# Performance work log

Hardware: AMD Instinct MI355X
Metric: run time of the kernel (lower is better)

The kernel has to match this reference:

```python
import jax, jax.numpy as jnp
import numpy as np

G, NB, C, K, R, S = 5, 5, 64, 3, 8, 2   # n_groups, n_blocks, n_feats, kernel, reduction, scale
MOCO = 256


def setup_inputs() -> dict:
    key = jax.random.key(0)
    ks = iter(jax.random.split(key, 32))
    def rn(shape, s=0.02):
        return jax.random.normal(next(ks), shape, jnp.float32) * s
    return {
        "x": jax.random.normal(next(ks), (16, 3, 64, 64), jnp.float32),
        "k_v": jax.random.normal(next(ks), (16, MOCO), jnp.float32),
        "head_w": rn((C, 3, K, K)), "head_b": rn((C,)),
        "comp_w": rn((C, MOCO)),
        # DA_conv params, stacked over [group, block, which-of-2]
        "da_kw1": rn((G, NB, 2, C, C)),
        "da_kw2": rn((G, NB, 2, C * K * K, C)),
        "da_cw": rn((G, NB, 2, C, C)), "da_cb": rn((G, NB, 2, C)),
        "ca_w1": rn((G, NB, 2, C // R, C)), "ca_w2": rn((G, NB, 2, C, C // R)),
        # DAB plain 3x3 convs (conv1, conv2)
        "dab_cw": rn((G, NB, 2, C, C, K, K)), "dab_cb": rn((G, NB, 2, C)),
        # per-group tail conv, body tail conv, upsampler, final conv
        "grp_w": rn((G, C, C, K, K)), "grp_b": rn((G, C)),
        "body_w": rn((C, C, K, K)), "body_b": rn((C,)),
        "up_w": rn((C * S * S, C, K, K)), "up_b": rn((C * S * S,)),
        "tail_w": rn((3, C, K, K)), "tail_b": rn((3,)),
    }


def lrelu(x):
    return jax.nn.leaky_relu(x, 0.1)


def conv2d(x, w, b):
    p = (K - 1) // 2
    y = jax.lax.conv_general_dilated(x, w, (1, 1), [(p, p), (p, p)],
                                     dimension_numbers=("NCHW", "OIHW", "NCHW"))
    return y + b[None, :, None, None]


def da_conv(x, kv, kw1, kw2, cw, cb, caw1, caw2):
    # x: [B,C,H,W], kv: [B,C]
    B, Ch, H, W = x.shape
    # per-sample, per-channel dynamic KxK kernel (torch: groups=B*C depthwise conv)
    ker = (lrelu(kv @ kw1.T) @ kw2.T).reshape(B, Ch, K, K)
    p = (K - 1) // 2
    xp = jnp.pad(x, ((0, 0), (0, 0), (p, p), (p, p)))
    out = jnp.zeros_like(x)
    for i in range(K):
        for j in range(K):
            out = out + ker[:, :, i, j, None, None] * xp[:, :, i:i + H, j:j + W]
    out = lrelu(out)
    # 1x1 conv (with bias)
    out = jnp.einsum("bchw,oc->bohw", out, cw) + cb[None, :, None, None]
    # CA gate on kv (two bias-free 1x1 convs on 1x1 spatial == matmuls)
    att = jax.nn.sigmoid(lrelu(kv @ caw1.T) @ caw2.T)  # [B,C]
    return out + x * att[:, :, None, None]


def pixel_shuffle(t, r):
    B, Ct, H, W = t.shape
    c = Ct // (r * r)
    return t.reshape(B, c, r, r, H, W).transpose(0, 1, 4, 2, 5, 3).reshape(B, c, H * r, W * r)


def _forward(x, k_v, head_w, head_b, comp_w, da_kw1, da_kw2, da_cw, da_cb,
             ca_w1, ca_w2, dab_cw, dab_cb, grp_w, grp_b, body_w, body_b,
             up_w, up_b, tail_w, tail_b):
    kv = lrelu(k_v @ comp_w.T)            # compress: [B, C]
    x0 = conv2d(x, head_w, head_b)        # head
    res = x0
    for g in range(G):                    # DAGs
        gin = res
        for n in range(NB):               # DABs
            bin_ = res
            out = lrelu(da_conv(res, kv, da_kw1[g, n, 0], da_kw2[g, n, 0],
                                da_cw[g, n, 0], da_cb[g, n, 0], ca_w1[g, n, 0], ca_w2[g, n, 0]))
            out = lrelu(conv2d(out, dab_cw[g, n, 0], dab_cb[g, n, 0]))
            out = lrelu(da_conv(out, kv, da_kw1[g, n, 1], da_kw2[g, n, 1],
                                da_cw[g, n, 1], da_cb[g, n, 1], ca_w1[g, n, 1], ca_w2[g, n, 1]))
            res = conv2d(out, dab_cw[g, n, 1], dab_cb[g, n, 1]) + bin_
        res = conv2d(res, grp_w[g], grp_b[g]) + gin
    res = conv2d(res, body_w, body_b) + x0
    t = pixel_shuffle(conv2d(res, up_w, up_b), S)   # Upsampler (scale=2)
    return conv2d(t, tail_w, tail_b)


def reference(x, k_v, head_w, head_b, comp_w, da_kw1, da_kw2, da_cw, da_cb,
              ca_w1, ca_w2, dab_cw, dab_cb, grp_w, grp_b, body_w, body_b,
              up_w, up_b, tail_w, tail_b):
    return _forward(x, k_v, head_w, head_b, comp_w, da_kw1, da_kw2, da_cw, da_cb,
                    ca_w1, ca_w2, dab_cw, dab_cb, grp_w, grp_b, body_w, body_b,
                    up_w, up_b, tail_w, tail_b)
```

## Files before the change

kernel.cpp:

```cpp
#include <hip/hip_runtime.h>
#include <math.h>

#define DEV __device__ __forceinline__

DEV float lrelu_f(float v) { return v > 0.f ? v : 0.1f * v; }

DEV unsigned short f2bf(float f) {
    unsigned u = __builtin_bit_cast(unsigned, f);
    unsigned r = u + 0x7FFFu + ((u >> 16) & 1u);
    return (unsigned short)(r >> 16);
}

DEV float bf2f(unsigned short s) {
    return __builtin_bit_cast(float, (unsigned)s << 16);
}

typedef __attribute__((ext_vector_type(8))) short bh8;
typedef __attribute__((ext_vector_type(16))) float f16acc;

#define MFMA32(acc, a, b) acc = __builtin_amdgcn_mfma_f32_32x32x16_bf16(a, b, acc, 0, 0, 0)

__global__ void transpose_w(const float* __restrict__ src, float* __restrict__ dst,
                            int L, int O, int KK) {
    int idx = blockIdx.x * 256 + threadIdx.x;
    int tot = L * O * KK;
    if (idx >= tot) return;
    int l = idx / (O * KK);
    int r = idx - l * (O * KK);
    int o = r / KK;
    int k = r - o * KK;
    dst[((size_t)l * KK + k) * O + o] = src[idx];
}

__global__ void pack3x3(const float* __restrict__ src, unsigned short* __restrict__ dst, int L) {
    int idx = blockIdx.x * 256 + threadIdx.x;
    if (idx >= L * 4608) return;
    int l = idx / 4608;
    int r = idx - l * 4608;
    int c = r >> 7;
    int rr = r & 127;
    int nt = rr >> 6, lane = rr & 63;
    int o = nt * 32 + (lane & 31);
    int kg = lane >> 5;
    unsigned short v[8];
#pragma unroll
    for (int j = 0; j < 8; ++j) {
        int k = c * 16 + kg * 8 + j;
        int t = k >> 6, cin = k & 63;
        v[j] = f2bf(src[(((size_t)l * 64 + o) * 64 + cin) * 9 + t]);
    }
    uint4 u;
    u.x = v[0] | ((unsigned)v[1] << 16);
    u.y = v[2] | ((unsigned)v[3] << 16);
    u.z = v[4] | ((unsigned)v[5] << 16);
    u.w = v[6] | ((unsigned)v[7] << 16);
    *(uint4*)(dst + (size_t)idx * 8) = u;
}

__global__ void pack_da(const float* __restrict__ src, unsigned short* __restrict__ dst, int L) {
    int idx = blockIdx.x * 256 + threadIdx.x;
    if (idx >= L * 512) return;
    int l = idx >> 9;
    int r = idx & 511;
    int c = r >> 7;
    int rr = r & 127;
    int nt = rr >> 6, lane = rr & 63;
    int o = nt * 32 + (lane & 31);
    int kg = lane >> 5;
    unsigned short v[8];
#pragma unroll
    for (int j = 0; j < 8; ++j) {
        int cin = c * 16 + kg * 8 + j;
        v[j] = f2bf(src[((size_t)l * 64 + o) * 64 + cin]);
    }
    uint4 u;
    u.x = v[0] | ((unsigned)v[1] << 16);
    u.y = v[2] | ((unsigned)v[3] << 16);
    u.z = v[4] | ((unsigned)v[5] << 16);
    u.w = v[6] | ((unsigned)v[7] << 16);
    *(uint4*)(dst + (size_t)idx * 8) = u;
}

__global__ void pack_up(const float* __restrict__ src, unsigned short* __restrict__ dst) {
    int idx = blockIdx.x * 256 + threadIdx.x;
    if (idx >= 18432) return;
    int c = idx >> 9;
    int nt = (idx >> 6) & 7;
    int lane = idx & 63;
    int o = nt * 32 + (lane & 31);
    int kg = lane >> 5;
    unsigned short v[8];
#pragma unroll
    for (int j = 0; j < 8; ++j) {
        int k = c * 16 + kg * 8 + j;
        int t = k >> 6, cin = k & 63;
        v[j] = f2bf(src[((size_t)o * 64 + cin) * 9 + t]);
    }
    uint4 u;
    u.x = v[0] | ((unsigned)v[1] << 16);
    u.y = v[2] | ((unsigned)v[3] << 16);
    u.z = v[4] | ((unsigned)v[5] << 16);
    u.w = v[6] | ((unsigned)v[7] << 16);
    *(uint4*)(dst + (size_t)idx * 8) = u;
}

__global__ void pack_tail(const float* __restrict__ src, unsigned short* __restrict__ dst) {
    int idx = blockIdx.x * 256 + threadIdx.x;
    if (idx >= 2304) return;
    int c = idx >> 6;
    int lane = idx & 63;
    int o = lane & 31;
    int kg = lane >> 5;
    unsigned short v[8];
#pragma unroll
    for (int j = 0; j < 8; ++j) {
        int k = c * 16 + kg * 8 + j;
        int t = k >> 6, cin = k & 63;
        v[j] = (o < 3) ? f2bf(src[((size_t)o * 64 + cin) * 9 + t]) : (unsigned short)0;
    }
    uint4 u;
    u.x = v[0] | ((unsigned)v[1] << 16);
    u.y = v[2] | ((unsigned)v[3] << 16);
    u.z = v[4] | ((unsigned)v[5] << 16);
    u.w = v[6] | ((unsigned)v[7] << 16);
    *(uint4*)(dst + (size_t)idx * 8) = u;
}

__global__ void kv_kernel(const float* __restrict__ kvin, const float* __restrict__ comp_w,
                          float* __restrict__ kv) {
    int b = blockIdx.x, c = threadIdx.x;
    const float* a = kvin + b * 256;
    const float* w = comp_w + c * 256;
    float s = 0.f;
    for (int m = 0; m < 256; ++m) s += a[m] * w[m];
    kv[b * 64 + c] = lrelu_f(s);
}

__global__ void kerprep(const float* __restrict__ kv, const float* __restrict__ kw1,
                        const float* __restrict__ kw2, const float* __restrict__ caw1,
                        const float* __restrict__ caw2, float* __restrict__ ker_all,
                        float* __restrict__ att_all) {
    int l = blockIdx.x >> 4;
    int b = blockIdx.x & 15;
    int c = threadIdx.x;
    __shared__ float kvb[64];
    __shared__ float t1[64];
    __shared__ float a1[8];
    kvb[c] = kv[b * 64 + c];
    __syncthreads();
    {
        const float* w1 = kw1 + (size_t)l * 4096 + c * 64;
        float s = 0.f;
        for (int j = 0; j < 64; ++j) s += kvb[j] * w1[j];
        t1[c] = lrelu_f(s);
    }
    if (c < 8) {
        const float* cw1 = caw1 + (size_t)l * 512 + c * 64;
        float s = 0.f;
        for (int j = 0; j < 64; ++j) s += kvb[j] * cw1[j];
        a1[c] = lrelu_f(s);
    }
    __syncthreads();
    const float* w2 = kw2 + (size_t)l * 576 * 64;
    for (int t = 0; t < 9; ++t) {
        const float* row = w2 + (size_t)(c * 9 + t) * 64;
        float s = 0.f;
        for (int j = 0; j < 64; ++j) s += t1[j] * row[j];
        ker_all[(((size_t)l * 16 + b) * 9 + t) * 64 + c] = s;
    }
    {
        const float* c2 = caw2 + (size_t)l * 512 + c * 8;
        float s = 0.f;
        for (int r = 0; r < 8; ++r) s += a1[r] * c2[r];
        att_all[((size_t)l * 16 + b) * 64 + c] = 1.f / (1.f + expf(-s));
    }
}

__global__ __launch_bounds__(256) void head_conv(const float* __restrict__ x,
                                                 const float* __restrict__ wt,
                                                 const float* __restrict__ bias,
                                                 float* __restrict__ x0,
                                                 float* __restrict__ res) {
    int t = threadIdx.x;
    int co = t & 63, q = t >> 6;
    int bid = blockIdx.x;
    int b = bid >> 7;
    int rem = bid & 127;
    int y = rem >> 1;
    int xs = (rem & 1) * 32 + q * 8;

    float bv = bias[co];
    float acc[8];
#pragma unroll
    for (int p = 0; p < 8; ++p) acc[p] = bv;

    int coff[10];
    bool cok[10];
#pragma unroll
    for (int i = 0; i < 10; ++i) {
        int col = xs - 1 + i;
        cok[i] = (col >= 0) && (col < 64);
        coff[i] = cok[i] ? col : 0;
    }
    for (int cin = 0; cin < 3; ++cin) {
#pragma unroll
        for (int ky = 0; ky < 3; ++ky) {
            int row = y + ky - 1;
            bool rok = (row >= 0) && (row < 64);
            const float* rp = x + ((size_t)(b * 3 + cin) * 64 + (rok ? row : 0)) * 64;
            float v[10];
#pragma unroll
            for (int i = 0; i < 10; ++i) v[i] = (rok && cok[i]) ? rp[coff[i]] : 0.f;
            const float* wp = wt + ((cin * 3 + ky) * 3) * 64 + co;
            float w0 = wp[0], w1 = wp[64], w2 = wp[128];
#pragma unroll
            for (int p = 0; p < 8; ++p) acc[p] += w0 * v[p] + w1 * v[p + 1] + w2 * v[p + 2];
        }
    }
    size_t ob = (((size_t)b * 64 + y) * 64 + xs) * 64 + co;
#pragma unroll
    for (int p = 0; p < 8; ++p) {
        x0[ob + (size_t)p * 64] = acc[p];
        res[ob + (size_t)p * 64] = acc[p];
    }
}

__global__ __launch_bounds__(256) void conv3x3_mfma(const float* __restrict__ in,
                                                    const unsigned short* __restrict__ wp,
                                                    const float* __restrict__ bias,
                                                    const float* __restrict__ resid,
                                                    float* __restrict__ out, int act) {
    __shared__ unsigned short sm[180 * 72];
    int tid = threadIdx.x;
    int bid = blockIdx.x;
    int b = bid >> 5;
    int rem = bid & 31;
    int ty = rem >> 2, tx = rem & 3;
    const float* inb = in + (size_t)b * 262144;

    for (int i = tid; i < 2880; i += 256) {
        int px = i >> 4, c4 = i & 15;
        int hy = px / 18, hx = px - hy * 18;
        int row = ty * 8 + hy - 1, col = tx * 16 + hx - 1;
        float4 v = make_float4(0.f, 0.f, 0.f, 0.f);
        if (row >= 0 && row < 64 && col >= 0 && col < 64)
            v = *(const float4*)(inb + (((size_t)row * 64 + col) * 64 + c4 * 4));
        uint2 u;
        u.x = f2bf(v.x) | ((unsigned)f2bf(v.y) << 16);
        u.y = f2bf(v.z) | ((unsigned)f2bf(v.w) << 16);
        *(uint2*)&sm[px * 72 + c4 * 4] = u;
    }
    __syncthreads();

    int lane = tid & 63, w = tid >> 6;
    int l31 = lane & 31, kg8 = (lane >> 5) * 8;
    int p0 = w * 32 + l31;
    int ly0 = p0 >> 4, lx0 = p0 & 15;

    f16acc a0 = {0,0,0,0,0,0,0,0,0,0,0,0,0,0,0,0};
    f16acc a1 = a0;

#pragma unroll
    for (int t = 0; t < 9; ++t) {
        int tyt = t / 3, txt = t - tyt * 3;
        int base = ((ly0 + tyt) * 18 + lx0 + txt) * 72 + kg8;
#pragma unroll
        for (int cc = 0; cc < 4; ++cc) {
            int c = t * 4 + cc;
            bh8 A = *(const bh8*)&sm[base + cc * 16];
            bh8 B0 = *(const bh8*)&wp[((size_t)(c * 2 + 0) * 64 + lane) * 8];
            bh8 B1 = *(const bh8*)&wp[((size_t)(c * 2 + 1) * 64 + lane) * 8];
            MFMA32(a0, A, B0);
            MFMA32(a1, A, B1);
        }
    }

    float bias0 = bias[l31], bias1 = bias[32 + l31];
    int hi = lane >> 5;
    size_t outb = (size_t)b * 262144;
#pragma unroll
    for (int r = 0; r < 16; ++r) {
        int rowm = (r & 3) + 8 * (r >> 2) + 4 * hi;
        int m = w * 32 + rowm;
        int gy = ty * 8 + (m >> 4), gx = tx * 16 + (m & 15);
        size_t i0 = outb + (((size_t)gy * 64 + gx) * 64);
        float v0 = a0[r] + bias0, v1 = a1[r] + bias1;
        if (resid) {
            v0 += resid[i0 + l31];
            v1 += resid[i0 + 32 + l31];
        }
        if (act) { v0 = lrelu_f(v0); v1 = lrelu_f(v1); }
        out[i0 + l31] = v0;
        out[i0 + 32 + l31] = v1;
    }
}

__global__ __launch_bounds__(256) void da_mfma(const float* __restrict__ in,
                                               const unsigned short* __restrict__ wp,
                                               const float* __restrict__ cb,
                                               const float* __restrict__ kerT,
                                               const float* __restrict__ attv,
                                               float* __restrict__ out) {
    __shared__ unsigned short sm[(180 + 128) * 72];
    const int MIDOFF = 180 * 72;
    int tid = threadIdx.x;
    int bid = blockIdx.x;
    int b = bid >> 5;
    int rem = bid & 31;
    int ty = rem >> 2, tx = rem & 3;
    const float* inb = in + (size_t)b * 262144;

    for (int i = tid; i < 2880; i += 256) {
        int px = i >> 4, c4 = i & 15;
        int hy = px / 18, hx = px - hy * 18;
        int row = ty * 8 + hy - 1, col = tx * 16 + hx - 1;
        float4 v = make_float4(0.f, 0.f, 0.f, 0.f);
        if (row >= 0 && row < 64 && col >= 0 && col < 64)
            v = *(const float4*)(inb + (((size_t)row * 64 + col) * 64 + c4 * 4));
        uint2 u;
        u.x = f2bf(v.x) | ((unsigned)f2bf(v.y) << 16);
        u.y = f2bf(v.z) | ((unsigned)f2bf(v.w) << 16);
        *(uint2*)&sm[px * 72 + c4 * 4] = u;
    }
    __syncthreads();

    {
        int c = tid & 63, q = tid >> 6;
        const float* kb = kerT + (size_t)b * 576;
        float k[9];
#pragma unroll
        for (int t = 0; t < 9; ++t) k[t] = kb[t * 64 + c];
#pragma unroll
        for (int rr = 0; rr < 2; ++rr) {
            int ly = q * 2 + rr;
            float m[16];
#pragma unroll
            for (int xx = 0; xx < 16; ++xx) m[xx] = 0.f;
#pragma unroll
            for (int ky = 0; ky < 3; ++ky) {
                int hr = ly + ky;
                float v[18];
#pragma unroll
                for (int i = 0; i < 18; ++i) v[i] = bf2f(sm[(hr * 18 + i) * 72 + c]);
                float k0 = k[ky * 3], k1 = k[ky * 3 + 1], k2 = k[ky * 3 + 2];
#pragma unroll
                for (int xx = 0; xx < 16; ++xx) m[xx] += k0 * v[xx] + k1 * v[xx + 1] + k2 * v[xx + 2];
            }
#pragma unroll
            for (int xx = 0; xx < 16; ++xx)
                sm[MIDOFF + (ly * 16 + xx) * 72 + c] = f2bf(lrelu_f(m[xx]));
        }
    }
    __syncthreads();

    int lane = tid & 63, w = tid >> 6;
    int l31 = lane & 31, kg8 = (lane >> 5) * 8;
    int base = MIDOFF + (w * 32 + l31) * 72 + kg8;

    f16acc a0 = {0,0,0,0,0,0,0,0,0,0,0,0,0,0,0,0};
    f16acc a1 = a0;
#pragma unroll
    for (int cc = 0; cc < 4; ++cc) {
        bh8 A = *(const bh8*)&sm[base + cc * 16];
        bh8 B0 = *(const bh8*)&wp[((size_t)(cc * 2 + 0) * 64 + lane) * 8];
        bh8 B1 = *(const bh8*)&wp[((size_t)(cc * 2 + 1) * 64 + lane) * 8];
        MFMA32(a0, A, B0);
        MFMA32(a1, A, B1);
    }

    float cb0 = cb[l31], cb1 = cb[32 + l31];
    float at0 = attv[b * 64 + l31], at1 = attv[b * 64 + 32 + l31];
    int hi = lane >> 5;
    size_t outb = (size_t)b * 262144;
#pragma unroll
    for (int r = 0; r < 16; ++r) {
        int rowm = (r & 3) + 8 * (r >> 2) + 4 * hi;
        int m = w * 32 + rowm;
        int gy = ty * 8 + (m >> 4), gx = tx * 16 + (m & 15);
        size_t i0 = outb + (((size_t)gy * 64 + gx) * 64);
        float v0 = a0[r] + cb0 + in[i0 + l31] * at0;
        float v1 = a1[r] + cb1 + in[i0 + 32 + l31] * at1;
        out[i0 + l31] = lrelu_f(v0);
        out[i0 + 32 + l31] = lrelu_f(v1);
    }
}

__global__ __launch_bounds__(256) void up_mfma(const float* __restrict__ in,
                                               const unsigned short* __restrict__ wp,
                                               const float* __restrict__ bias,
                                               float* __restrict__ shuf) {
    __shared__ unsigned short sm[100 * 72];
    int tid = threadIdx.x;
    int bid = blockIdx.x;
    int b = bid >> 6;
    int t6 = bid & 63;
    int ty = t6 >> 3, tx = t6 & 7;
    const float* inb = in + (size_t)b * 262144;

    for (int i = tid; i < 1600; i += 256) {
        int px = i >> 4, c4 = i & 15;
        int hy = px / 10, hx = px - hy * 10;
        int row = ty * 8 + hy - 1, col = tx * 8 + hx - 1;
        float4 v = make_float4(0.f, 0.f, 0.f, 0.f);
        if (row >= 0 && row < 64 && col >= 0 && col < 64)
            v = *(const float4*)(inb + (((size_t)row * 64 + col) * 64 + c4 * 4));
        uint2 u;
        u.x = f2bf(v.x) | ((unsigned)f2bf(v.y) << 16);
        u.y = f2bf(v.z) | ((unsigned)f2bf(v.w) << 16);
        *(uint2*)&sm[px * 72 + c4 * 4] = u;
    }
    __syncthreads();

    int lane = tid & 63, w = tid >> 6;
    int l31 = lane & 31, kg8 = (lane >> 5) * 8;
    int ly0 = l31 >> 3, lx0 = l31 & 7;

    f16acc a00 = {0,0,0,0,0,0,0,0,0,0,0,0,0,0,0,0};
    f16acc a01 = a00, a10 = a00, a11 = a00;

#pragma unroll
    for (int t = 0; t < 9; ++t) {
        int tyt = t / 3, txt = t - tyt * 3;
        int base0 = ((ly0 + tyt) * 10 + lx0 + txt) * 72 + kg8;
        int base1 = base0 + 2880;
#pragma unroll
        for (int cc = 0; cc < 4; ++cc) {
            int c = t * 4 + cc;
            bh8 A0 = *(const bh8*)&sm[base0 + cc * 16];
            bh8 A1 = *(const bh8*)&sm[base1 + cc * 16];
            bh8 B0 = *(const bh8*)&wp[((size_t)(c * 8 + w * 2 + 0) * 64 + lane) * 8];
            bh8 B1 = *(const bh8*)&wp[((size_t)(c * 8 + w * 2 + 1) * 64 + lane) * 8];
            MFMA32(a00, A0, B0);
            MFMA32(a01, A0, B1);
            MFMA32(a10, A1, B0);
            MFMA32(a11, A1, B1);
        }
    }

    int co0 = w * 64 + l31, co1 = co0 + 32;
    float bias0 = bias[co0], bias1 = bias[co1];
    int ch0 = co0 >> 2, r10 = (co0 >> 1) & 1, r20 = co0 & 1;
    int ch1 = co1 >> 2, r11 = (co1 >> 1) & 1, r21 = co1 & 1;
    int hi = lane >> 5;
#pragma unroll
    for (int r = 0; r < 16; ++r) {
        int rowm = (r & 3) + 8 * (r >> 2) + 4 * hi;
#pragma unroll
        for (int mt = 0; mt < 2; ++mt) {
            int m = mt * 32 + rowm;
            int y = ty * 8 + (m >> 3), x = tx * 8 + (m & 7);
            float va = (mt == 0) ? a00[r] : a10[r];
            float vb = (mt == 0) ? a01[r] : a11[r];
            shuf[(((size_t)b * 128 + 2 * y + r10) * 128 + 2 * x + r20) * 64 + ch0] = va + bias0;
            shuf[(((size_t)b * 128 + 2 * y + r11) * 128 + 2 * x + r21) * 64 + ch1] = vb + bias1;
        }
    }
}

__global__ __launch_bounds__(256) void tail_mfma(const float* __restrict__ shuf,
                                                 const unsigned short* __restrict__ wp,
                                                 const float* __restrict__ bias,
                                                 float* __restrict__ outp) {
    __shared__ unsigned short sm[324 * 72];
    int tid = threadIdx.x;
    int bid = blockIdx.x;
    int b = bid >> 6;
    int rem = bid & 63;
    int ty = rem >> 3, tx = rem & 7;
    const float* sb = shuf + (size_t)b * 128 * 128 * 64;

    for (int i = tid; i < 5184; i += 256) {
        int px = i >> 4, c4 = i & 15;
        int hy = px / 18, hx = px - hy * 18;
        int row = ty * 16 + hy - 1, col = tx * 16 + hx - 1;
        float4 v = make_float4(0.f, 0.f, 0.f, 0.f);
        if (row >= 0 && row < 128 && col >= 0 && col < 128)
            v = *(const float4*)(sb + (((size_t)row * 128 + col) * 64 + c4 * 4));
        uint2 u;
        u.x = f2bf(v.x) | ((unsigned)f2bf(v.y) << 16);
        u.y = f2bf(v.z) | ((unsigned)f2bf(v.w) << 16);
        *(uint2*)&sm[px * 72 + c4 * 4] = u;
    }
    __syncthreads();

    int lane = tid & 63, w = tid >> 6;
    int l31 = lane & 31, kg8 = (lane >> 5) * 8;
    int mbase = w * 64;
    int p0 = mbase + l31;
    int ly0 = p0 >> 4, lx0 = p0 & 15;

    f16acc a0 = {0,0,0,0,0,0,0,0,0,0,0,0,0,0,0,0};
    f16acc a1 = a0;

#pragma unroll
    for (int t = 0; t < 9; ++t) {
        int tyt = t / 3, txt = t - tyt * 3;
        int base0 = ((ly0 + tyt) * 18 + lx0 + txt) * 72 + kg8;
        int base1 = base0 + 2592;
#pragma unroll
        for (int cc = 0; cc < 4; ++cc) {
            int c = t * 4 + cc;
            bh8 A0 = *(const bh8*)&sm[base0 + cc * 16];
            bh8 A1 = *(const bh8*)&sm[base1 + cc * 16];
            bh8 B = *(const bh8*)&wp[((size_t)c * 64 + lane) * 8];
            MFMA32(a0, A0, B);
            MFMA32(a1, A1, B);
        }
    }

    if (l31 < 3) {
        float bv = bias[l31];
        int hi = lane >> 5;
        size_t ob = ((size_t)b * 3 + l31) * 16384;
#pragma unroll
        for (int r = 0; r < 16; ++r) {
            int rowm = (r & 3) + 8 * (r >> 2) + 4 * hi;
            int m0 = mbase + rowm;
            int gy0 = ty * 16 + (m0 >> 4), gx0 = tx * 16 + (m0 & 15);
            outp[ob + (size_t)gy0 * 128 + gx0] = a0[r] + bv;
            int m1 = m0 + 32;
            int gy1 = ty * 16 + (m1 >> 4), gx1 = tx * 16 + (m1 & 15);
            outp[ob + (size_t)gy1 * 128 + gx1] = a1[r] + bv;
        }
    }
}

extern "C" void kernel_launch(void* const* d_in, const int* in_sizes, int n_in,
                              void* d_out, int out_size, void* d_ws, size_t ws_size,
                              hipStream_t stream) {
    const float* x      = (const float*)d_in[0];
    const float* k_v    = (const float*)d_in[1];
    const float* head_w = (const float*)d_in[2];
    const float* head_b = (const float*)d_in[3];
    const float* comp_w = (const float*)d_in[4];
    const float* da_kw1 = (const float*)d_in[5];
    const float* da_kw2 = (const float*)d_in[6];
    const float* da_cw  = (const float*)d_in[7];
    const float* da_cb  = (const float*)d_in[8];
    const float* ca_w1  = (const float*)d_in[9];
    const float* ca_w2  = (const float*)d_in[10];
    const float* dab_cw = (const float*)d_in[11];
    const float* dab_cb = (const float*)d_in[12];
    const float* grp_w  = (const float*)d_in[13];
    const float* grp_b  = (const float*)d_in[14];
    const float* body_w = (const float*)d_in[15];
    const float* body_b = (const float*)d_in[16];
    const float* up_w   = (const float*)d_in[17];
    const float* up_b   = (const float*)d_in[18];
    const float* tail_w = (const float*)d_in[19];
    const float* tail_b = (const float*)d_in[20];

    char* base = (char*)d_ws;
    auto alloc = [&](size_t bytes) -> char* {
        char* p = base;
        base += (bytes + 255) & ~(size_t)255;
        return p;
    };
    unsigned short* wp_dab  = (unsigned short*)alloc((size_t)50 * 36864 * 2);
    unsigned short* wp_grp  = (unsigned short*)alloc((size_t)5 * 36864 * 2);
    unsigned short* wp_body = (unsigned short*)alloc((size_t)36864 * 2);
    unsigned short* wp_up   = (unsigned short*)alloc((size_t)147456 * 2);
    unsigned short* wp_da   = (unsigned short*)alloc((size_t)50 * 4096 * 2);
    unsigned short* wp_tail = (unsigned short*)alloc((size_t)18432 * 2);
    float* wT_head = (float*)alloc(1728 * 4);
    float* kvbuf   = (float*)alloc(1024 * 4);
    float* ker_all = (float*)alloc((size_t)460800 * 4);
    float* att_all = (float*)alloc((size_t)51200 * 4);
    const size_t ACT = (size_t)16 * 64 * 64 * 64;
    float* x0  = (float*)alloc(ACT * 4);
    float* b0  = (float*)alloc(ACT * 4);
    float* b1  = (float*)alloc(ACT * 4);
    float* b2  = (float*)alloc(ACT * 4);
    float* t0b = (float*)alloc(ACT * 4);
    float* t1b = (float*)alloc(ACT * 4);
    float* shuf = (float*)alloc((size_t)16 * 128 * 128 * 64 * 4);

    pack3x3<<<900, 256, 0, stream>>>(dab_cw, wp_dab, 50);
    pack3x3<<<90, 256, 0, stream>>>(grp_w, wp_grp, 5);
    pack3x3<<<18, 256, 0, stream>>>(body_w, wp_body, 1);
    pack_da<<<100, 256, 0, stream>>>(da_cw, wp_da, 50);
    pack_up<<<72, 256, 0, stream>>>(up_w, wp_up);
    pack_tail<<<9, 256, 0, stream>>>(tail_w, wp_tail);
    transpose_w<<<7, 256, 0, stream>>>(head_w, wT_head, 1, 64, 27);

    kv_kernel<<<16, 64, 0, stream>>>(k_v, comp_w, kvbuf);
    kerprep<<<800, 64, 0, stream>>>(kvbuf, da_kw1, da_kw2, ca_w1, ca_w2, ker_all, att_all);

    head_conv<<<2048, 256, 0, stream>>>(x, wT_head, head_b, x0, b0);

    for (int g = 0; g < 5; ++g) {
        float* rin = b0;
        for (int n = 0; n < 5; ++n) {
            int l0 = (g * 5 + n) * 2, l1 = l0 + 1;
            da_mfma<<<512, 256, 0, stream>>>(rin, wp_da + (size_t)l0 * 4096,
                                             da_cb + (size_t)l0 * 64, ker_all + (size_t)l0 * 9216,
                                             att_all + (size_t)l0 * 1024, t0b);
            conv3x3_mfma<<<512, 256, 0, stream>>>(t0b, wp_dab + (size_t)l0 * 36864,
                                                  dab_cb + (size_t)l0 * 64, nullptr, t1b, 1);
            da_mfma<<<512, 256, 0, stream>>>(t1b, wp_da + (size_t)l1 * 4096,
                                             da_cb + (size_t)l1 * 64, ker_all + (size_t)l1 * 9216,
                                             att_all + (size_t)l1 * 1024, t0b);
            float* rout = (rin == b1) ? b2 : b1;
            conv3x3_mfma<<<512, 256, 0, stream>>>(t0b, wp_dab + (size_t)l1 * 36864,
                                                  dab_cb + (size_t)l1 * 64, rin, rout, 0);
            rin = rout;
        }
        float* gout = (rin == b1) ? b2 : b1;
        conv3x3_mfma<<<512, 256, 0, stream>>>(rin, wp_grp + (size_t)g * 36864,
                                              grp_b + (size_t)g * 64, b0, gout, 0);
        float* ob0 = b0;
        b0 = gout;
        b1 = ob0;
        b2 = rin;
    }
    conv3x3_mfma<<<512, 256, 0, stream>>>(b0, wp_body, body_b, x0, b1, 0);

    up_mfma<<<1024, 256, 0, stream>>>(b1, wp_up, up_b, shuf);
    tail_mfma<<<1024, 256, 0, stream>>>(shuf, wp_tail, tail_b, (float*)d_out);
}
```

Measured before the change: 1.887 ms.

## Store intermediate activations as bf16 and enlarge conv3x3 tiles to 16x16

Intermediate activations between kernels are now written and read as bf16, with fp32 copies kept only for residual streams. This halves global memory traffic and removes the per-load fp32-to-bf16 conversion in every conv, DA, upsample and tail kernel. conv3x3_mfma now computes a 16x16 tile per block with four accumulators per wave, so each B-fragment load is reused twice and half as many blocks are launched. The DA kernel also stages its 1x1 weights in LDS. Rounding intermediates to bf16 adds precision loss, and fewer blocks may lower occupancy.

```diff
diff --git a/kernel.cpp b/kernel.cpp
--- a/kernel.cpp
+++ b/kernel.cpp
@@ -180,7 +180,8 @@
                                                  const float* __restrict__ wt,
                                                  const float* __restrict__ bias,
                                                  float* __restrict__ x0,
-                                                 float* __restrict__ res) {
+                                                 float* __restrict__ res,
+                                                 unsigned short* __restrict__ resS) {
     int t = threadIdx.x;
     int co = t & 63, q = t >> 6;
     int bid = blockIdx.x;
@@ -222,60 +223,179 @@
     for (int p = 0; p < 8; ++p) {
         x0[ob + (size_t)p * 64] = acc[p];
         res[ob + (size_t)p * 64] = acc[p];
-    }
-}
-
-__global__ __launch_bounds__(256) void conv3x3_mfma(const float* __restrict__ in,
+        resS[ob + (size_t)p * 64] = f2bf(acc[p]);
+    }
+}
+
+__global__ __launch_bounds__(256) void conv3x3_mfma(const unsigned short* __restrict__ in,
                                                     const unsigned short* __restrict__ wp,
                                                     const float* __restrict__ bias,
-                                                    const float* __restrict__ resid,
-                                                    float* __restrict__ out, int act) {
+                                                    const float* __restrict__ residF,
+                                                    float* __restrict__ outF,
+                                                    unsigned short* __restrict__ outB,
+                                                    int act) {
+    __shared__ unsigned short sm[324 * 72];
+    int tid = threadIdx.x;
+    int bid = blockIdx.x;
+    int b = bid >> 4, ty = (bid >> 2) & 3, tx = bid & 3;
+    const unsigned short* inb = in + (size_t)b * 262144;
+
+    for (int i = tid; i < 2592; i += 256) {
+        int px = i >> 3, c8 = i & 7;
+        int hy = px / 18, hx = px - hy * 18;
+        int row = ty * 16 + hy - 1, col = tx * 16 + hx - 1;
+        uint4 u = make_uint4(0u, 0u, 0u, 0u);
+        if (row >= 0 && row < 64 && col >= 0 && col < 64)
+            u = *(const uint4*)(inb + (((size_t)row * 64 + col) * 64 + c8 * 8));
+        *(uint4*)&sm[px * 72 + c8 * 8] = u;
+    }
+    __syncthreads();
+
+    int lane = tid & 63, w = tid >> 6;
+    int l31 = lane & 31, kg8 = (lane >> 5) * 8;
+    int mbase = w * 64;
+    int p0 = mbase + l31;
+    int ly0 = p0 >> 4, lx0 = p0 & 15;
+
+    f16acc a00 = {0,0,0,0,0,0,0,0,0,0,0,0,0,0,0,0};
+    f16acc a01 = a00, a10 = a00, a11 = a00;
+
+#pragma unroll
+    for (int t = 0; t < 9; ++t) {
+        int tyt = t / 3, txt = t - tyt * 3;
+        int base0 = ((ly0 + tyt) * 18 + lx0 + txt) * 72 + kg8;
+        int base1 = base0 + 2592;
+#pragma unroll
+        for (int cc = 0; cc < 4; ++cc) {
+            int c = t * 4 + cc;
+            bh8 A0 = *(const bh8*)&sm[base0 + cc * 16];
+            bh8 A1 = *(const bh8*)&sm[base1 + cc * 16];
+            bh8 B0 = *(const bh8*)&wp[((size_t)(c * 2 + 0) * 64 + lane) * 8];
+            bh8 B1 = *(const bh8*)&wp[((size_t)(c * 2 + 1) * 64 + lane) * 8];
+            MFMA32(a00, A0, B0);
+            MFMA32(a01, A0, B1);
+            MFMA32(a10, A1, B0);
+            MFMA32(a11, A1, B1);
+        }
+    }
+
+    float bias0 = bias[l31], bias1 = bias[32 + l31];
+    int hi = lane >> 5;
+    size_t outb = (size_t)b * 262144;
+#pragma unroll
+    for (int r = 0; r < 16; ++r) {
+        int rowm = (r & 3) + 8 * (r >> 2) + 4 * hi;
+        int m0 = mbase + rowm;
+        int gy0 = ty * 16 + (m0 >> 4), gx0 = tx * 16 + (m0 & 15);
+        size_t i0 = outb + (((size_t)gy0 * 64 + gx0) * 64);
+        int m1 = m0 + 32;
+        int gy1 = ty * 16 + (m1 >> 4), gx1 = tx * 16 + (m1 & 15);
+        size_t i1 = outb + (((size_t)gy1 * 64 + gx1) * 64);
+        float v00 = a00[r] + bias0, v01 = a01[r] + bias1;
+        float v10 = a10[r] + bias0, v11 = a11[r] + bias1;
+        if (residF) {
+            v00 += residF[i0 + l31];
+            v01 += residF[i0 + 32 + l31];
+            v10 += residF[i1 + l31];
+            v11 += residF[i1 + 32 + l31];
+        }
+        if (act) {
+            v00 = lrelu_f(v00); v01 = lrelu_f(v01);
+            v10 = lrelu_f(v10); v11 = lrelu_f(v11);
+        }
+        if (outF) {
+            outF[i0 + l31] = v00;
+            outF[i0 + 32 + l31] = v01;
+            outF[i1 + l31] = v10;
+            outF[i1 + 32 + l31] = v11;
+        }
+        if (outB) {
+            outB[i0 + l31] = f2bf(v00);
+            outB[i0 + 32 + l31] = f2bf(v01);
+            outB[i1 + l31] = f2bf(v10);
+            outB[i1 + 32 + l31] = f2bf(v11);
+        }
+    }
+}
+
+__global__ __launch_bounds__(256) void da_mfma(const unsigned short* __restrict__ in,
+                                               const unsigned short* __restrict__ wp,
+                                               const float* __restrict__ cb,
+                                               const float* __restrict__ kerT,
+                                               const float* __restrict__ attv,
+                                               unsigned short* __restrict__ out) {
     __shared__ unsigned short sm[180 * 72];
+    __shared__ unsigned short mid[128 * 72];
+    __shared__ unsigned short bds[4096];
     int tid = threadIdx.x;
     int bid = blockIdx.x;
     int b = bid >> 5;
     int rem = bid & 31;
     int ty = rem >> 2, tx = rem & 3;
-    const float* inb = in + (size_t)b * 262144;
-
-    for (int i = tid; i < 2880; i += 256) {
-        int px = i >> 4, c4 = i & 15;
+    const unsigned short* inb = in + (size_t)b * 262144;
+
+    for (int i = tid; i < 1440; i += 256) {
+        int px = i >> 3, c8 = i & 7;
         int hy = px / 18, hx = px - hy * 18;
         int row = ty * 8 + hy - 1, col = tx * 16 + hx - 1;
-        float4 v = make_float4(0.f, 0.f, 0.f, 0.f);
+        uint4 u = make_uint4(0u, 0u, 0u, 0u);
         if (row >= 0 && row < 64 && col >= 0 && col < 64)
-            v = *(const float4*)(inb + (((size_t)row * 64 + col) * 64 + c4 * 4));
-        uint2 u;
-        u.x = f2bf(v.x) | ((unsigned)f2bf(v.y) << 16);
-        u.y = f2bf(v.z) | ((unsigned)f2bf(v.w) << 16);
-        *(uint2*)&sm[px * 72 + c4 * 4] = u;
+            u = *(const uint4*)(inb + (((size_t)row * 64 + col) * 64 + c8 * 8));
+        *(uint4*)&sm[px * 72 + c8 * 8] = u;
+    }
+#pragma unroll
+    for (int i = 0; i < 2; ++i) {
+        int idx = i * 256 + tid;
+        *(uint4*)&bds[idx * 8] = *(const uint4*)&wp[idx * 8];
+    }
+    __syncthreads();
+
+    {
+        int c = tid & 63, q = tid >> 6;
+        const float* kb = kerT + (size_t)b * 576;
+        float k[9];
+#pragma unroll
+        for (int t = 0; t < 9; ++t) k[t] = kb[t * 64 + c];
+#pragma unroll
+        for (int rr = 0; rr < 2; ++rr) {
+            int ly = q * 2 + rr;
+            float m[16];
+#pragma unroll
+            for (int xx = 0; xx < 16; ++xx) m[xx] = 0.f;
+#pragma unroll
+            for (int ky = 0; ky < 3; ++ky) {
+                int hr = ly + ky;
+                float v[18];
+#pragma unroll
+                for (int i = 0; i < 18; ++i) v[i] = bf2f(sm[(hr * 18 + i) * 72 + c]);
+                float k0 = k[ky * 3], k1 = k[ky * 3 + 1], k2 = k[ky * 3 + 2];
+#pragma unroll
+                for (int xx = 0; xx < 16; ++xx) m[xx] += k0 * v[xx] + k1 * v[xx + 1] + k2 * v[xx + 2];
+            }
+#pragma unroll
+            for (int xx = 0; xx < 16; ++xx)
+                mid[(ly * 16 + xx) * 72 + c] = f2bf(lrelu_f(m[xx]));
+        }
     }
     __syncthreads();
 
     int lane = tid & 63, w = tid >> 6;
     int l31 = lane & 31, kg8 = (lane >> 5) * 8;
-    int p0 = w * 32 + l31;
-    int ly0 = p0 >> 4, lx0 = p0 & 15;
+    int base = (w * 32 + l31) * 72 + kg8;
 
     f16acc a0 = {0,0,0,0,0,0,0,0,0,0,0,0,0,0,0,0};
     f16acc a1 = a0;
-
-#pragma unroll
-    for (int t = 0; t < 9; ++t) {
-        int tyt = t / 3, txt = t - tyt * 3;
-        int base = ((ly0 + tyt) * 18 + lx0 + txt) * 72 + kg8;
-#pragma unroll
-        for (int cc = 0; cc < 4; ++cc) {
-            int c = t * 4 + cc;
-            bh8 A = *(const bh8*)&sm[base + cc * 16];
-            bh8 B0 = *(const bh8*)&wp[((size_t)(c * 2 + 0) * 64 + lane) * 8];
-            bh8 B1 = *(const bh8*)&wp[((size_t)(c * 2 + 1) * 64 + lane) * 8];
-            MFMA32(a0, A, B0);
-            MFMA32(a1, A, B1);
-        }
-    }
-
-    float bias0 = bias[l31], bias1 = bias[32 + l31];
+#pragma unroll
+    for (int cc = 0; cc < 4; ++cc) {
+        bh8 A = *(const bh8*)&mid[base + cc * 16];
+        bh8 B0 = *(const bh8*)&bds[((cc * 2 + 0) * 64 + lane) * 8];
+        bh8 B1 = *(const bh8*)&bds[((cc * 2 + 1) * 64 + lane) * 8];
+        MFMA32(a0, A, B0);
+        MFMA32(a1, A, B1);
+    }
+
+    float cb0 = cb[l31], cb1 = cb[32 + l31];
+    float at0 = attv[b * 64 + l31], at1 = attv[b * 64 + 32 + l31];
     int hi = lane >> 5;
     size_t outb = (size_t)b * 262144;
 #pragma unroll
@@ -284,130 +404,33 @@
         int m = w * 32 + rowm;
         int gy = ty * 8 + (m >> 4), gx = tx * 16 + (m & 15);
         size_t i0 = outb + (((size_t)gy * 64 + gx) * 64);
-        float v0 = a0[r] + bias0, v1 = a1[r] + bias1;
-        if (resid) {
-            v0 += resid[i0 + l31];
-            v1 += resid[i0 + 32 + l31];
-        }
-        if (act) { v0 = lrelu_f(v0); v1 = lrelu_f(v1); }
-        out[i0 + l31] = v0;
-        out[i0 + 32 + l31] = v1;
-    }
-}
-
-__global__ __launch_bounds__(256) void da_mfma(const float* __restrict__ in,
-                                               const unsigned short* __restrict__ wp,
-                                               const float* __restrict__ cb,
-                                               const float* __restrict__ kerT,
-                                               const float* __restrict__ attv,
-                                               float* __restrict__ out) {
-    __shared__ unsigned short sm[(180 + 128) * 72];
-    const int MIDOFF = 180 * 72;
-    int tid = threadIdx.x;
-    int bid = blockIdx.x;
-    int b = bid >> 5;
-    int rem = bid & 31;
-    int ty = rem >> 2, tx = rem & 3;
-    const float* inb = in + (size_t)b * 262144;
-
-    for (int i = tid; i < 2880; i += 256) {
-        int px = i >> 4, c4 = i & 15;
-        int hy = px / 18, hx = px - hy * 18;
-        int row = ty * 8 + hy - 1, col = tx * 16 + hx - 1;
-        float4 v = make_float4(0.f, 0.f, 0.f, 0.f);
-        if (row >= 0 && row < 64 && col >= 0 && col < 64)
-            v = *(const float4*)(inb + (((size_t)row * 64 + col) * 64 + c4 * 4));
-        uint2 u;
-        u.x = f2bf(v.x) | ((unsigned)f2bf(v.y) << 16);
-        u.y = f2bf(v.z) | ((unsigned)f2bf(v.w) << 16);
-        *(uint2*)&sm[px * 72 + c4 * 4] = u;
-    }
-    __syncthreads();
-
-    {
-        int c = tid & 63, q = tid >> 6;
-        const float* kb = kerT + (size_t)b * 576;
-        float k[9];
-#pragma unroll
-        for (int t = 0; t < 9; ++t) k[t] = kb[t * 64 + c];
-#pragma unroll
-        for (int rr = 0; rr < 2; ++rr) {
-            int ly = q * 2 + rr;
-            float m[16];
-#pragma unroll
-            for (int xx = 0; xx < 16; ++xx) m[xx] = 0.f;
-#pragma unroll
-            for (int ky = 0; ky < 3; ++ky) {
-                int hr = ly + ky;
-                float v[18];
-#pragma unroll
-                for (int i = 0; i < 18; ++i) v[i] = bf2f(sm[(hr * 18 + i) * 72 + c]);
-                float k0 = k[ky * 3], k1 = k[ky * 3 + 1], k2 = k[ky * 3 + 2];
-#pragma unroll
-                for (int xx = 0; xx < 16; ++xx) m[xx] += k0 * v[xx] + k1 * v[xx + 1] + k2 * v[xx + 2];
-            }
-#pragma unroll
-            for (int xx = 0; xx < 16; ++xx)
-                sm[MIDOFF + (ly * 16 + xx) * 72 + c] = f2bf(lrelu_f(m[xx]));
-        }
-    }
-    __syncthreads();
-
-    int lane = tid & 63, w = tid >> 6;
-    int l31 = lane & 31, kg8 = (lane >> 5) * 8;
-    int base = MIDOFF + (w * 32 + l31) * 72 + kg8;
-
-    f16acc a0 = {0,0,0,0,0,0,0,0,0,0,0,0,0,0,0,0};
-    f16acc a1 = a0;
-#pragma unroll
-    for (int cc = 0; cc < 4; ++cc) {
-        bh8 A = *(const bh8*)&sm[base + cc * 16];
-        bh8 B0 = *(const bh8*)&wp[((size_t)(cc * 2 + 0) * 64 + lane) * 8];
-        bh8 B1 = *(const bh8*)&wp[((size_t)(cc * 2 + 1) * 64 + lane) * 8];
-        MFMA32(a0, A, B0);
-        MFMA32(a1, A, B1);
-    }
-
-    float cb0 = cb[l31], cb1 = cb[32 + l31];
-    float at0 = attv[b * 64 + l31], at1 = attv[b * 64 + 32 + l31];
-    int hi = lane >> 5;
-    size_t outb = (size_t)b * 262144;
-#pragma unroll
-    for (int r = 0; r < 16; ++r) {
-        int rowm = (r & 3) + 8 * (r >> 2) + 4 * hi;
-        int m = w * 32 + rowm;
-        int gy = ty * 8 + (m >> 4), gx = tx * 16 + (m & 15);
-        size_t i0 = outb + (((size_t)gy * 64 + gx) * 64);
-        float v0 = a0[r] + cb0 + in[i0 + l31] * at0;
-        float v1 = a1[r] + cb1 + in[i0 + 32 + l31] * at1;
-        out[i0 + l31] = lrelu_f(v0);
-        out[i0 + 32 + l31] = lrelu_f(v1);
-    }
-}
-
-__global__ __launch_bounds__(256) void up_mfma(const float* __restrict__ in,
+        float v0 = a0[r] + cb0 + bf2f(in[i0 + l31]) * at0;
+        float v1 = a1[r] + cb1 + bf2f(in[i0 + 32 + l31]) * at1;
+        out[i0 + l31] = f2bf(lrelu_f(v0));
+        out[i0 + 32 + l31] = f2bf(lrelu_f(v1));
+    }
+}
+
+__global__ __launch_bounds__(256) void up_mfma(const unsigned short* __restrict__ in,
                                                const unsigned short* __restrict__ wp,
                                                const float* __restrict__ bias,
-                                               float* __restrict__ shuf) {
+                                               unsigned short* __restrict__ shuf) {
     __shared__ unsigned short sm[100 * 72];
     int tid = threadIdx.x;
     int bid = blockIdx.x;
     int b = bid >> 6;
     int t6 = bid & 63;
     int ty = t6 >> 3, tx = t6 & 7;
-    const float* inb = in + (size_t)b * 262144;
-
-    for (int i = tid; i < 1600; i += 256) {
-        int px = i >> 4, c4 = i & 15;
+    const unsigned short* inb = in + (size_t)b * 262144;
+
+    for (int i = tid; i < 800; i += 256) {
+        int px = i >> 3, c8 = i & 7;
         int hy = px / 10, hx = px - hy * 10;
         int row = ty * 8 + hy - 1, col = tx * 8 + hx - 1;
-        float4 v = make_float4(0.f, 0.f, 0.f, 0.f);
+        uint4 u = make_uint4(0u, 0u, 0u, 0u);
         if (row >= 0 && row < 64 && col >= 0 && col < 64)
-            v = *(const float4*)(inb + (((size_t)row * 64 + col) * 64 + c4 * 4));
-        uint2 u;
-        u.x = f2bf(v.x) | ((unsigned)f2bf(v.y) << 16);
-        u.y = f2bf(v.z) | ((unsigned)f2bf(v.w) << 16);
-        *(uint2*)&sm[px * 72 + c4 * 4] = u;
+            u = *(const uint4*)(inb + (((size_t)row * 64 + col) * 64 + c8 * 8));
+        *(uint4*)&sm[px * 72 + c8 * 8] = u;
     }
     __syncthreads();
 
@@ -451,13 +474,13 @@
             int y = ty * 8 + (m >> 3), x = tx * 8 + (m & 7);
             float va = (mt == 0) ? a00[r] : a10[r];
             float vb = (mt == 0) ? a01[r] : a11[r];
-            shuf[(((size_t)b * 128 + 2 * y + r10) * 128 + 2 * x + r20) * 64 + ch0] = va + bias0;
-            shuf[(((size_t)b * 128 + 2 * y + r11) * 128 + 2 * x + r21) * 64 + ch1] = vb + bias1;
-        }
-    }
-}
-
-__global__ __launch_bounds__(256) void tail_mfma(const float* __restrict__ shuf,
+            shuf[(((size_t)b * 128 + 2 * y + r10) * 128 + 2 * x + r20) * 64 + ch0] = f2bf(va + bias0);
+            shuf[(((size_t)b * 128 + 2 * y + r11) * 128 + 2 * x + r21) * 64 + ch1] = f2bf(vb + bias1);
+        }
+    }
+}
+
+__global__ __launch_bounds__(256) void tail_mfma(const unsigned short* __restrict__ shuf,
                                                  const unsigned short* __restrict__ wp,
                                                  const float* __restrict__ bias,
                                                  float* __restrict__ outp) {
@@ -467,19 +490,16 @@
     int b = bid >> 6;
     int rem = bid & 63;
     int ty = rem >> 3, tx = rem & 7;
-    const float* sb = shuf + (size_t)b * 128 * 128 * 64;
-
-    for (int i = tid; i < 5184; i += 256) {
-        int px = i >> 4, c4 = i & 15;
+    const unsigned short* sb = shuf + (size_t)b * 128 * 128 * 64;
+
+    for (int i = tid; i < 2592; i += 256) {
+        int px = i >> 3, c8 = i & 7;
         int hy = px / 18, hx = px - hy * 18;
         int row = ty * 16 + hy - 1, col = tx * 16 + hx - 1;
-        float4 v = make_float4(0.f, 0.f, 0.f, 0.f);
+        uint4 u = make_uint4(0u, 0u, 0u, 0u);
         if (row >= 0 && row < 128 && col >= 0 && col < 128)
-            v = *(const float4*)(sb + (((size_t)row * 128 + col) * 64 + c4 * 4));
-        uint2 u;
-        u.x = f2bf(v.x) | ((unsigned)f2bf(v.y) << 16);
-        u.y = f2bf(v.z) | ((unsigned)f2bf(v.w) << 16);
-        *(uint2*)&sm[px * 72 + c4 * 4] = u;
+            u = *(const uint4*)(sb + (((size_t)row * 128 + col) * 64 + c8 * 8));
+        *(uint4*)&sm[px * 72 + c8 * 8] = u;
     }
     __syncthreads();
 
@@ -567,13 +587,16 @@
     float* ker_all = (float*)alloc((size_t)460800 * 4);
     float* att_all = (float*)alloc((size_t)51200 * 4);
     const size_t ACT = (size_t)16 * 64 * 64 * 64;
-    float* x0  = (float*)alloc(ACT * 4);
-    float* b0  = (float*)alloc(ACT * 4);
-    float* b1  = (float*)alloc(ACT * 4);
-    float* b2  = (float*)alloc(ACT * 4);
-    float* t0b = (float*)alloc(ACT * 4);
-    float* t1b = (float*)alloc(ACT * 4);
-    float* shuf = (float*)alloc((size_t)16 * 128 * 128 * 64 * 4);
+    float* x0 = (float*)alloc(ACT * 4);
+    float* rA = (float*)alloc(ACT * 4);
+    float* rB = (float*)alloc(ACT * 4);
+    float* rC = (float*)alloc(ACT * 4);
+    unsigned short* sA = (unsigned short*)alloc(ACT * 2);
+    unsigned short* sB = (unsigned short*)alloc(ACT * 2);
+    unsigned short* sC = (unsigned short*)alloc(ACT * 2);
+    unsigned short* t0 = (unsigned short*)alloc(ACT * 2);
+    unsigned short* t1 = (unsigned short*)alloc(ACT * 2);
+    unsigned short* shuf = (unsigned short*)alloc((size_t)16 * 128 * 128 * 64 * 2);
 
     pack3x3<<<900, 256, 0, stream>>>(dab_cw, wp_dab, 50);
     pack3x3<<<90, 256, 0, stream>>>(grp_w, wp_grp, 5);
@@ -586,35 +609,37 @@
     kv_kernel<<<16, 64, 0, stream>>>(k_v, comp_w, kvbuf);
     kerprep<<<800, 64, 0, stream>>>(kvbuf, da_kw1, da_kw2, ca_w1, ca_w2, ker_all, att_all);
 
-    head_conv<<<2048, 256, 0, stream>>>(x, wT_head, head_b, x0, b0);
+    head_conv<<<2048, 256, 0, stream>>>(x, wT_head, head_b, x0, rA, sA);
 
     for (int g = 0; g < 5; ++g) {
-        float* rin = b0;
+        float* curF = rA;
+        unsigned short* curS = sA;
         for (int n = 0; n < 5; ++n) {
             int l0 = (g * 5 + n) * 2, l1 = l0 + 1;
-            da_mfma<<<512, 256, 0, stream>>>(rin, wp_da + (size_t)l0 * 4096,
+            da_mfma<<<512, 256, 0, stream>>>(curS, wp_da + (size_t)l0 * 4096,
                                              da_cb + (size_t)l0 * 64, ker_all + (size_t)l0 * 9216,
-                                             att_all + (size_t)l0 * 1024, t0b);
-            conv3x3_mfma<<<512, 256, 0, stream>>>(t0b, wp_dab + (size_t)l0 * 36864,
-                                                  dab_cb + (size_t)l0 * 64, nullptr, t1b, 1);
-            da_mfma<<<512, 256, 0, stream>>>(t1b, wp_da + (size_t)l1 * 4096,
+                                             att_all + (size_t)l0 * 1024, t0);
+            conv3x3_mfma<<<256, 256, 0, stream>>>(t0, wp_dab + (size_t)l0 * 36864,
+                                                  dab_cb + (size_t)l0 * 64, nullptr,
+                                                  nullptr, t1, 1);
+            da_mfma<<<512, 256, 0, stream>>>(t1, wp_da + (size_t)l1 * 4096,
                                              da_cb + (size_t)l1 * 64, ker_all + (size_t)l1 * 9216,
-                                             att_all + (size_t)l1 * 1024, t0b);
-            float* rout = (rin == b1) ? b2 : b1;
-            conv3x3_mfma<<<512, 256, 0, stream>>>(t0b, wp_dab + (size_t)l1 * 36864,
-                                                  dab_cb + (size_t)l1 * 64, rin, rout, 0);
-            rin = rout;
-        }
-        float* gout = (rin == b1) ? b2 : b1;
-        conv3x3_mfma<<<512, 256, 0, stream>>>(rin, wp_grp + (size_t)g * 36864,
-                                              grp_b + (size_t)g * 64, b0, gout, 0);
-        float* ob0 = b0;
-        b0 = gout;
-        b1 = ob0;
-        b2 = rin;
-    }
-    conv3x3_mfma<<<512, 256, 0, stream>>>(b0, wp_body, body_b, x0, b1, 0);
-
-    up_mfma<<<1024, 256, 0, stream>>>(b1, wp_up, up_b, shuf);
+                                             att_all + (size_t)l1 * 1024, t0);
+            float* outF = (curF == rB) ? rC : rB;
+            unsigned short* outS = (curS == sB) ? sC : sB;
+            conv3x3_mfma<<<256, 256, 0, stream>>>(t0, wp_dab + (size_t)l1 * 36864,
+                                                  dab_cb + (size_t)l1 * 64, curF,
+                                                  outF, outS, 0);
+            curF = outF;
+            curS = outS;
+        }
+        conv3x3_mfma<<<256, 256, 0, stream>>>(curS, wp_grp + (size_t)g * 36864,
+                                              grp_b + (size_t)g * 64, rA, rC, sC, 0);
+        float* tf = rA; rA = rC; rC = tf;
+        unsigned short* ts = sA; sA = sC; sC = ts;
+    }
+    conv3x3_mfma<<<256, 256, 0, stream>>>(sA, wp_body, body_b, x0, nullptr, t0, 0);
+
+    up_mfma<<<1024, 256, 0, stream>>>(t0, wp_up, up_b, shuf);
     tail_mfma<<<1024, 256, 0, stream>>>(shuf, wp_tail, tail_b, (float*)d_out);
 }
```

Result: slower. 1.966 ms (+4.2%).
